# Kernel tuning notes

Hardware: AMD Instinct MI355X
Metric: run time of the kernel (lower is better)

The kernel has to match this reference:

```python
import jax, jax.numpy as jnp
import numpy as np

N = 50000      # num nodes
IN = 256       # in_channels
H = 4          # heads
C = 64         # out_channels per head (concat=False -> out_dim = C)
HOPS = 3       # max_hops == num hops provided
E = 400000     # edges per hop
NEG_SLOPE = 0.2


def setup_inputs() -> dict:
    key = jax.random.key(0)
    ks = jax.random.split(key, 10)
    s_in = 1.0 / np.sqrt(IN)
    s_c = 1.0 / np.sqrt(C)
    return {
        "x": jax.random.normal(ks[0], (N, IN), jnp.float32),
        "ei0": jax.random.randint(ks[1], (2, E), 0, N, dtype=jnp.int32),
        "ei1": jax.random.randint(ks[2], (2, E), 0, N, dtype=jnp.int32),
        "ei2": jax.random.randint(ks[3], (2, E), 0, N, dtype=jnp.int32),
        # shared left/right projections (lin_l / lin_r, shared across hops)
        "W_l": jax.random.normal(ks[4], (IN, H * C), jnp.float32) * s_in,
        "b_l": jnp.zeros((H * C,), jnp.float32),
        "W_r": jax.random.normal(ks[5], (IN, H * C), jnp.float32) * s_in,
        "b_r": jnp.zeros((H * C,), jnp.float32),
        # hop-specific attention vectors and output biases
        "att": jax.random.normal(ks[6], (HOPS, H, C), jnp.float32) * s_c,
        "bias": jnp.zeros((HOPS, C), jnp.float32),
        # hop gate (single Linear since gate_hidden=None)
        "W_gate": jax.random.normal(ks[7], (IN, HOPS), jnp.float32) * s_in,
        "b_gate": jnp.zeros((HOPS,), jnp.float32),
    }


def _segment_softmax(logits, seg, n):
    # logits: [E, H], seg: [E] destination node ids
    m = jax.ops.segment_max(logits, seg, num_segments=n)          # [N, H]
    m = jnp.where(jnp.isfinite(m), m, 0.0)                        # empty segments -> 0
    ex = jnp.exp(logits - m[seg])
    s = jax.ops.segment_sum(ex, seg, num_segments=n)              # [N, H]
    return ex / (s[seg] + 1e-16)


def _gatv2_hop(x_l, x_r, edge_index, att_k, bias_k):
    # x_l, x_r: [N, H, C] shared projections; edge_index: [2, Ek]
    src, dst = edge_index[0], edge_index[1]
    s = jax.nn.leaky_relu(x_l[src] + x_r[dst], NEG_SLOPE)         # [Ek, H, C]
    alpha = jnp.einsum("ehc,hc->eh", s, att_k)                    # [Ek, H]
    alpha = _segment_softmax(alpha, dst, N)
    msg = jax.ops.segment_sum(x_l[src] * alpha[..., None], dst, num_segments=N)  # [N, H, C]
    return msg.mean(axis=1) + bias_k                              # concat=False -> head mean, [N, C]


def reference(x, ei0, ei1, ei2, W_l, b_l, W_r, b_r, att, bias, W_gate, b_gate):
    # shared projections computed once
    x_l = (x @ W_l + b_l).reshape(N, H, C)
    x_r = (x @ W_r + b_r).reshape(N, H, C)

    # hop 0 gets self-loops (add_self_loops=True); higher hops do not
    ar = jnp.arange(N, dtype=ei0.dtype)
    ei0_sl = jnp.concatenate([ei0, jnp.stack([ar, ar])], axis=1)
    edges = [ei0_sl, ei1, ei2]

    messages = jnp.stack(
        [_gatv2_hop(x_l, x_r, edges[k], att[k], bias[k]) for k in range(HOPS)],
        axis=1,
    )  # [N, HOPS, C]

    logits = x @ W_gate + b_gate                                  # [N, HOPS]
    weights = jax.nn.softmax(logits, axis=-1)
    out = jnp.einsum("nkc,nk->nc", messages, weights)             # [N, C]
    return out
```

## Files before the change

kernel.cpp:

```cpp
#include <hip/hip_runtime.h>
#include <math.h>

#define N_NODES 50000
#define IN_DIM 256
#define HEADS 4
#define CDIM 64
#define HC 256
#define HOPS 3
#define EDGES 400000
#define NEG_SLOPE 0.2f
#define SEG (EDGES + N_NODES)
#define TOT_E (3 * EDGES + N_NODES)
#define CAP 40

#define NB_GATE  ((N_NODES + 3) / 4)
#define NB_PACKW ((IN_DIM * 2 * HC) / 256)
#define NB_SCAT  ((TOT_E + 255) / 256)
#define GEMM_BX  ((N_NODES + 127) / 128)

typedef unsigned short ushort;
using short8  = __attribute__((ext_vector_type(8))) short;
using floatx4 = __attribute__((ext_vector_type(4))) float;
using f32x2   = __attribute__((ext_vector_type(2))) float;

__device__ __forceinline__ void decode_flat(int f, int& k, int& e)
{
    if (f < SEG)              { k = 0; e = f; }
    else if (f < SEG + EDGES) { k = 1; e = f - SEG; }
    else                      { k = 2; e = f - SEG - EDGES; }
}

__device__ __forceinline__ ushort f2bf(float f)
{
    unsigned u = __float_as_uint(f);
    unsigned r = u + 0x7fffu + ((u >> 16) & 1u);
    return (ushort)(r >> 16);
}

__device__ __forceinline__ f32x2 bf2x(unsigned u)
{
    f32x2 r;
    r.x = __uint_as_float(u << 16);
    r.y = __uint_as_float(u & 0xffff0000u);
    return r;
}

__device__ __forceinline__ f32x2 lrelu2(f32x2 v)
{
    return __builtin_elementwise_max(v, 0.2f * v);
}

__global__ __launch_bounds__(256) void prep(
    const float* __restrict__ X, const float* __restrict__ Wg,
    const float* __restrict__ bg, float* __restrict__ gw,
    ushort* __restrict__ Xb,
    const float* __restrict__ Wl, const float* __restrict__ Wr,
    ushort* __restrict__ WT,
    const int* __restrict__ ei0, const int* __restrict__ ei1,
    const int* __restrict__ ei2, int* __restrict__ cnt,
    int* __restrict__ bucket)
{
    const int blk = blockIdx.x;
    const int tid = threadIdx.x;

    if (blk < NB_GATE) {
        const int node = (blk * 256 + tid) >> 6;
        const int lane = tid & 63;
        if (node >= N_NODES) return;

        float4 xv = ((const float4*)(X + (size_t)node * IN_DIM))[lane];

        union { ushort s[4]; uint2 u; } o;
        o.s[0] = f2bf(xv.x); o.s[1] = f2bf(xv.y);
        o.s[2] = f2bf(xv.z); o.s[3] = f2bf(xv.w);
        ((uint2*)(Xb + (size_t)node * IN_DIM))[lane] = o.u;

        float a0 = 0.f, a1 = 0.f, a2 = 0.f;
        const int i0 = lane * 4;
        a0 += xv.x * Wg[(i0 + 0) * HOPS + 0]; a1 += xv.x * Wg[(i0 + 0) * HOPS + 1]; a2 += xv.x * Wg[(i0 + 0) * HOPS + 2];
        a0 += xv.y * Wg[(i0 + 1) * HOPS + 0]; a1 += xv.y * Wg[(i0 + 1) * HOPS + 1]; a2 += xv.y * Wg[(i0 + 1) * HOPS + 2];
        a0 += xv.z * Wg[(i0 + 2) * HOPS + 0]; a1 += xv.z * Wg[(i0 + 2) * HOPS + 1]; a2 += xv.z * Wg[(i0 + 2) * HOPS + 2];
        a0 += xv.w * Wg[(i0 + 3) * HOPS + 0]; a1 += xv.w * Wg[(i0 + 3) * HOPS + 1]; a2 += xv.w * Wg[(i0 + 3) * HOPS + 2];

        #pragma unroll
        for (int off = 32; off >= 1; off >>= 1) {
            a0 += __shfl_xor(a0, off);
            a1 += __shfl_xor(a1, off);
            a2 += __shfl_xor(a2, off);
        }
        if (lane == 0) {
            float l0 = a0 + bg[0], l1 = a1 + bg[1], l2 = a2 + bg[2];
            float m = fmaxf(l0, fmaxf(l1, l2));
            float e0 = expf(l0 - m), e1 = expf(l1 - m), e2 = expf(l2 - m);
            float inv = 1.f / (e0 + e1 + e2);
            gw[node * HOPS + 0] = e0 * inv;
            gw[node * HOPS + 1] = e1 * inv;
            gw[node * HOPS + 2] = e2 * inv;
        }
    } else if (blk < NB_GATE + NB_PACKW) {
        int id = (blk - NB_GATE) * 256 + tid;
        int n = id >> 8;
        int k = id & 255;
        float v = (n < HC) ? Wl[k * HC + n] : Wr[k * HC + (n - HC)];
        WT[(size_t)n * IN_DIM + k] = f2bf(v);
    } else {
        int f = (blk - NB_GATE - NB_PACKW) * 256 + tid;
        if (f >= TOT_E) return;
        int k, e; decode_flat(f, k, e);
        int s, d;
        if (k == 0 && e >= EDGES) { s = d = e - EDGES; }
        else {
            const int* ei = (k == 0) ? ei0 : (k == 1) ? ei1 : ei2;
            s = ei[e]; d = ei[EDGES + e];
        }
        int pos = atomicAdd(&cnt[k * N_NODES + d], 1);
        if (pos < CAP)
            bucket[((size_t)k * N_NODES + d) * CAP + pos] = s;
    }
}

#define TM 128
#define TN 128
#define TK 32
#define LDP 40

__global__ __launch_bounds__(256) void gemm_mfma(
    const ushort* __restrict__ Xb, const ushort* __restrict__ WT,
    const float* __restrict__ b_l, const float* __restrict__ b_r,
    ushort* __restrict__ xlb, ushort* __restrict__ xrb, int M)
{
    __shared__ ushort As[TM][LDP];
    __shared__ ushort Bs[TN][LDP];
    const int tid  = threadIdx.x;
    const int wave = tid >> 6, lane = tid & 63;
    const int row0 = blockIdx.x * TM;
    const int col0 = blockIdx.y * TN;
    const int wy = (wave >> 1) * 64, wx = (wave & 1) * 64;
    const int lrow = lane & 15, lk = (lane >> 4) * 8;

    floatx4 acc[4][4];
    #pragma unroll
    for (int i = 0; i < 4; i++)
        #pragma unroll
        for (int j = 0; j < 4; j++)
            acc[i][j] = (floatx4){0.f, 0.f, 0.f, 0.f};

    for (int k0 = 0; k0 < IN_DIM; k0 += TK) {
        #pragma unroll
        for (int j = 0; j < 2; j++) {
            int id = tid + 256 * j;
            int r  = id >> 2;
            int c  = (id & 3) * 8;
            int gr = row0 + r;
            uint4 v = make_uint4(0u, 0u, 0u, 0u);
            if (gr < M)
                v = *(const uint4*)(Xb + (size_t)gr * IN_DIM + k0 + c);
            *(uint4*)&As[r][c] = v;
        }
        #pragma unroll
        for (int j = 0; j < 2; j++) {
            int id = tid + 256 * j;
            int r  = id >> 2;
            int c  = (id & 3) * 8;
            *(uint4*)&Bs[r][c] =
                *(const uint4*)(WT + (size_t)(col0 + r) * IN_DIM + k0 + c);
        }
        __syncthreads();

        short8 af[4], bf[4];
        #pragma unroll
        for (int mi = 0; mi < 4; mi++)
            af[mi] = *(const short8*)&As[wy + mi * 16 + lrow][lk];
        #pragma unroll
        for (int ni = 0; ni < 4; ni++)
            bf[ni] = *(const short8*)&Bs[wx + ni * 16 + lrow][lk];

        #pragma unroll
        for (int mi = 0; mi < 4; mi++)
            #pragma unroll
            for (int ni = 0; ni < 4; ni++)
                acc[mi][ni] = __builtin_amdgcn_mfma_f32_16x16x32_bf16(
                    bf[ni], af[mi], acc[mi][ni], 0, 0, 0);
        __syncthreads();
    }

    const int csub = (lane >> 4) * 4;
    #pragma unroll
    for (int mi = 0; mi < 4; mi++) {
        int grow = row0 + wy + mi * 16 + lrow;
        if (grow < M) {
            #pragma unroll
            for (int ni = 0; ni < 4; ni++) {
                int gcol = col0 + wx + ni * 16 + csub;
                floatx4 v = acc[mi][ni];
                const bool left = (gcol < HC);
                const float4 b = left ? *(const float4*)(b_l + gcol)
                                      : *(const float4*)(b_r + gcol - HC);
                union { ushort s[4]; uint2 u; } o;
                o.s[0] = f2bf(v[0] + b.x);
                o.s[1] = f2bf(v[1] + b.y);
                o.s[2] = f2bf(v[2] + b.z);
                o.s[3] = f2bf(v[3] + b.w);
                ushort* dst = left ? (xlb + (size_t)grow * HC + gcol)
                                   : (xrb + (size_t)grow * HC + gcol - HC);
                *(uint2*)dst = o.u;
            }
        }
    }
}

__global__ __launch_bounds__(256) void node_all(
    const ushort* __restrict__ xlb, const ushort* __restrict__ xrb,
    const int* __restrict__ cnt, const int* __restrict__ bucket,
    const float* __restrict__ att, const float* __restrict__ gw,
    const float* __restrict__ bias, float* __restrict__ out)
{
    const int n    = blockIdx.x * 4 + (threadIdx.x >> 6);
    const int lane = threadIdx.x & 63;
    if (n >= N_NODES) return;
    const int half = lane >> 5;
    const int sub  = lane & 31;
    const unsigned laneoff = (unsigned)sub * 8;

    uint4 rq = *(const uint4*)(xrb + (size_t)n * HC + laneoff);
    f32x2 rr[4] = { bf2x(rq.x), bf2x(rq.y), bf2x(rq.z), bf2x(rq.w) };

    f32x2 outacc[4] = { {0.f,0.f}, {0.f,0.f}, {0.f,0.f}, {0.f,0.f} };

    #pragma unroll
    for (int k = 0; k < HOPS; ++k) {
        const int deg = min(cnt[k * N_NODES + n], CAP);
        const int* bk = bucket + ((size_t)k * N_NODES + n) * CAP;

        const float4 a0 = ((const float4*)(att + (size_t)k * HC))[sub * 2 + 0];
        const float4 a1 = ((const float4*)(att + (size_t)k * HC))[sub * 2 + 1];
        f32x2 w2[4] = { {a0.x, a0.y}, {a0.z, a0.w}, {a1.x, a1.y}, {a1.z, a1.w} };

        float denom = 0.f;
        f32x2 acc2[4] = { {0.f,0.f}, {0.f,0.f}, {0.f,0.f}, {0.f,0.f} };

        if (deg > 0) {
            const int degm1 = deg - 1;
            int myS = (lane < deg) ? bk[lane] : 0;
            const int npair = (deg + 1) >> 1;

            int s0 = __shfl(myS, min(half, degm1));
            uint4 q = *(const uint4*)(xlb + (unsigned)s0 * HC + laneoff);

            for (int j = 0; j < npair; j++) {
                int sn = __shfl(myS, min(2 * (j + 1) + half, degm1));
                uint4 qn = *(const uint4*)(xlb + (unsigned)sn * HC + laneoff);

                f32x2 f0 = bf2x(q.x), f1 = bf2x(q.y);
                f32x2 f2 = bf2x(q.z), f3 = bf2x(q.w);

                f32x2 pp = w2[0] * lrelu2(f0 + rr[0]);
                pp = __builtin_elementwise_fma(w2[1], lrelu2(f1 + rr[1]), pp);
                pp = __builtin_elementwise_fma(w2[2], lrelu2(f2 + rr[2]), pp);
                pp = __builtin_elementwise_fma(w2[3], lrelu2(f3 + rr[3]), pp);
                float p = pp.x + pp.y;

                p += __shfl_xor(p, 1);
                p += __shfl_xor(p, 2);
                p += __shfl_xor(p, 4);

                bool valid = (2 * j + half) < deg;
                float ex = valid ? __expf(p) : 0.f;
                denom += ex;
                f32x2 ex2 = { ex, ex };
                acc2[0] = __builtin_elementwise_fma(ex2, f0, acc2[0]);
                acc2[1] = __builtin_elementwise_fma(ex2, f1, acc2[1]);
                acc2[2] = __builtin_elementwise_fma(ex2, f2, acc2[2]);
                acc2[3] = __builtin_elementwise_fma(ex2, f3, acc2[3]);
                q = qn;
            }
        }

        denom += __shfl_xor(denom, 32);
        const float inv = (denom > 0.f) ? 1.f / denom : 0.f;
        #pragma unroll
        for (int i = 0; i < 4; i++) {
            acc2[i].x += __shfl_xor(acc2[i].x, 32);
            acc2[i].y += __shfl_xor(acc2[i].y, 32);
            acc2[i].x *= inv;
            acc2[i].y *= inv;
            acc2[i].x += __shfl_xor(acc2[i].x, 8);
            acc2[i].y += __shfl_xor(acc2[i].y, 8);
            acc2[i].x += __shfl_xor(acc2[i].x, 16);
            acc2[i].y += __shfl_xor(acc2[i].y, 16);
        }

        const float g   = gw[n * HOPS + k];
        const float s   = g * 0.25f;
        const f32x2 s2  = { s, s };
        const f32x2 g2  = { g, g };
        const f32x2* bb2 =
            (const f32x2*)(bias + (size_t)k * CDIM + (size_t)(sub & 7) * 8);
        #pragma unroll
        for (int i = 0; i < 4; i++) {
            outacc[i] = __builtin_elementwise_fma(s2, acc2[i], outacc[i]);
            outacc[i] = __builtin_elementwise_fma(g2, bb2[i], outacc[i]);
        }
    }

    if (lane < 8) {
        float4 o0 = { outacc[0].x, outacc[0].y, outacc[1].x, outacc[1].y };
        float4 o1 = { outacc[2].x, outacc[2].y, outacc[3].x, outacc[3].y };
        float4* dst = (float4*)(out + (size_t)n * CDIM + (size_t)lane * 8);
        dst[0] = o0;
        dst[1] = o1;
    }
}

extern "C" void kernel_launch(void* const* d_in, const int* in_sizes, int n_in,
                              void* d_out, int out_size, void* d_ws, size_t ws_size,
                              hipStream_t stream)
{
    const float* x      = (const float*)d_in[0];
    const int*   ei0    = (const int*)d_in[1];
    const int*   ei1    = (const int*)d_in[2];
    const int*   ei2    = (const int*)d_in[3];
    const float* W_l    = (const float*)d_in[4];
    const float* b_l    = (const float*)d_in[5];
    const float* W_r    = (const float*)d_in[6];
    const float* b_r    = (const float*)d_in[7];
    const float* att    = (const float*)d_in[8];
    const float* bias   = (const float*)d_in[9];
    const float* W_gate = (const float*)d_in[10];
    const float* b_gate = (const float*)d_in[11];

    const size_t NHC = (size_t)N_NODES * HC;
    float* ws      = (float*)d_ws;
    float* gwbuf   = ws;
    int*   cnt     = (int*)(gwbuf + HOPS * N_NODES);
    int*   bucket  = cnt + HOPS * N_NODES;
    ushort* xlb    = (ushort*)(bucket + (size_t)HOPS * N_NODES * CAP);
    ushort* xrb    = xlb + NHC;
    ushort* Xb     = xrb + NHC;
    ushort* WT     = Xb + NHC;

    hipMemsetAsync(cnt, 0, (size_t)HOPS * N_NODES * sizeof(int), stream);

    prep<<<NB_GATE + NB_PACKW + NB_SCAT, 256, 0, stream>>>(
        x, W_gate, b_gate, gwbuf, Xb, W_l, W_r, WT,
        ei0, ei1, ei2, cnt, bucket);

    dim3 ggrid(GEMM_BX, 4);
    gemm_mfma<<<ggrid, 256, 0, stream>>>(Xb, WT, b_l, b_r, xlb, xrb, N_NODES);

    node_all<<<(N_NODES + 3) / 4, 256, 0, stream>>>(
        xlb, xrb, cnt, bucket, att, gwbuf, bias, (float*)d_out);
}
```

Baseline: 406.4 us.

## Split node aggregation across hops: one wave per hop, combine via LDS

The per-node kernel now launches one 192-thread block per node, with each of the three waves handling one hop's attention and aggregation in parallel instead of looping over hops serially within one wave. Per-hop gated results are written to shared memory and summed after a block barrier, then stored with one coalesced write per node. This shortens each wave's dependent gather chain and exposes more memory-level parallelism. The cost is a block barrier, more blocks, a redundant load of the right-projection row in every wave, and uneven work when hop degrees differ.

```diff
diff --git a/kernel.cpp b/kernel.cpp
--- a/kernel.cpp
+++ b/kernel.cpp
@@ -209,107 +209,95 @@
     }
 }
 
-__global__ __launch_bounds__(256) void node_all(
+__global__ __launch_bounds__(192) void node_all(
     const ushort* __restrict__ xlb, const ushort* __restrict__ xrb,
     const int* __restrict__ cnt, const int* __restrict__ bucket,
     const float* __restrict__ att, const float* __restrict__ gw,
     const float* __restrict__ bias, float* __restrict__ out)
 {
-    const int n    = blockIdx.x * 4 + (threadIdx.x >> 6);
+    __shared__ float lds[HOPS][CDIM];
+    const int n    = blockIdx.x;
+    const int k    = threadIdx.x >> 6;
     const int lane = threadIdx.x & 63;
-    if (n >= N_NODES) return;
     const int half = lane >> 5;
     const int sub  = lane & 31;
     const unsigned laneoff = (unsigned)sub * 8;
 
+    const int deg = min(cnt[k * N_NODES + n], CAP);
+    const int* bk = bucket + ((size_t)k * N_NODES + n) * CAP;
+
     uint4 rq = *(const uint4*)(xrb + (size_t)n * HC + laneoff);
     f32x2 rr[4] = { bf2x(rq.x), bf2x(rq.y), bf2x(rq.z), bf2x(rq.w) };
 
-    f32x2 outacc[4] = { {0.f,0.f}, {0.f,0.f}, {0.f,0.f}, {0.f,0.f} };
+    const float4 a0 = ((const float4*)(att + (size_t)k * HC))[sub * 2 + 0];
+    const float4 a1 = ((const float4*)(att + (size_t)k * HC))[sub * 2 + 1];
+    f32x2 w2[4] = { {a0.x, a0.y}, {a0.z, a0.w}, {a1.x, a1.y}, {a1.z, a1.w} };
+
+    float denom = 0.f;
+    f32x2 acc2[4] = { {0.f,0.f}, {0.f,0.f}, {0.f,0.f}, {0.f,0.f} };
+
+    if (deg > 0) {
+        const int degm1 = deg - 1;
+        int myS = (lane < deg) ? bk[lane] : 0;
+        const int npair = (deg + 1) >> 1;
+
+        int s0 = __shfl(myS, min(half, degm1));
+        uint4 q = *(const uint4*)(xlb + (unsigned)s0 * HC + laneoff);
+
+        for (int j = 0; j < npair; j++) {
+            int sn = __shfl(myS, min(2 * (j + 1) + half, degm1));
+            uint4 qn = *(const uint4*)(xlb + (unsigned)sn * HC + laneoff);
+
+            f32x2 f0 = bf2x(q.x), f1 = bf2x(q.y);
+            f32x2 f2 = bf2x(q.z), f3 = bf2x(q.w);
+
+            f32x2 pp = w2[0] * lrelu2(f0 + rr[0]);
+            pp = __builtin_elementwise_fma(w2[1], lrelu2(f1 + rr[1]), pp);
+            pp = __builtin_elementwise_fma(w2[2], lrelu2(f2 + rr[2]), pp);
+            pp = __builtin_elementwise_fma(w2[3], lrelu2(f3 + rr[3]), pp);
+            float p = pp.x + pp.y;
+
+            p += __shfl_xor(p, 1);
+            p += __shfl_xor(p, 2);
+            p += __shfl_xor(p, 4);
+
+            bool valid = (2 * j + half) < deg;
+            float ex = valid ? __expf(p) : 0.f;
+            denom += ex;
+            f32x2 ex2 = { ex, ex };
+            acc2[0] = __builtin_elementwise_fma(ex2, f0, acc2[0]);
+            acc2[1] = __builtin_elementwise_fma(ex2, f1, acc2[1]);
+            acc2[2] = __builtin_elementwise_fma(ex2, f2, acc2[2]);
+            acc2[3] = __builtin_elementwise_fma(ex2, f3, acc2[3]);
+            q = qn;
+        }
+    }
+
+    denom += __shfl_xor(denom, 32);
+    const float inv = (denom > 0.f) ? 1.f / denom : 0.f;
+    const float g   = gw[n * HOPS + k];
+    const float* bb = bias + (size_t)k * CDIM + (size_t)(sub & 7) * 8;
 
     #pragma unroll
-    for (int k = 0; k < HOPS; ++k) {
-        const int deg = min(cnt[k * N_NODES + n], CAP);
-        const int* bk = bucket + ((size_t)k * N_NODES + n) * CAP;
-
-        const float4 a0 = ((const float4*)(att + (size_t)k * HC))[sub * 2 + 0];
-        const float4 a1 = ((const float4*)(att + (size_t)k * HC))[sub * 2 + 1];
-        f32x2 w2[4] = { {a0.x, a0.y}, {a0.z, a0.w}, {a1.x, a1.y}, {a1.z, a1.w} };
-
-        float denom = 0.f;
-        f32x2 acc2[4] = { {0.f,0.f}, {0.f,0.f}, {0.f,0.f}, {0.f,0.f} };
-
-        if (deg > 0) {
-            const int degm1 = deg - 1;
-            int myS = (lane < deg) ? bk[lane] : 0;
-            const int npair = (deg + 1) >> 1;
-
-            int s0 = __shfl(myS, min(half, degm1));
-            uint4 q = *(const uint4*)(xlb + (unsigned)s0 * HC + laneoff);
-
-            for (int j = 0; j < npair; j++) {
-                int sn = __shfl(myS, min(2 * (j + 1) + half, degm1));
-                uint4 qn = *(const uint4*)(xlb + (unsigned)sn * HC + laneoff);
-
-                f32x2 f0 = bf2x(q.x), f1 = bf2x(q.y);
-                f32x2 f2 = bf2x(q.z), f3 = bf2x(q.w);
-
-                f32x2 pp = w2[0] * lrelu2(f0 + rr[0]);
-                pp = __builtin_elementwise_fma(w2[1], lrelu2(f1 + rr[1]), pp);
-                pp = __builtin_elementwise_fma(w2[2], lrelu2(f2 + rr[2]), pp);
-                pp = __builtin_elementwise_fma(w2[3], lrelu2(f3 + rr[3]), pp);
-                float p = pp.x + pp.y;
-
-                p += __shfl_xor(p, 1);
-                p += __shfl_xor(p, 2);
-                p += __shfl_xor(p, 4);
-
-                bool valid = (2 * j + half) < deg;
-                float ex = valid ? __expf(p) : 0.f;
-                denom += ex;
-                f32x2 ex2 = { ex, ex };
-                acc2[0] = __builtin_elementwise_fma(ex2, f0, acc2[0]);
-                acc2[1] = __builtin_elementwise_fma(ex2, f1, acc2[1]);
-                acc2[2] = __builtin_elementwise_fma(ex2, f2, acc2[2]);
-                acc2[3] = __builtin_elementwise_fma(ex2, f3, acc2[3]);
-                q = qn;
-            }
-        }
-
-        denom += __shfl_xor(denom, 32);
-        const float inv = (denom > 0.f) ? 1.f / denom : 0.f;
-        #pragma unroll
-        for (int i = 0; i < 4; i++) {
-            acc2[i].x += __shfl_xor(acc2[i].x, 32);
-            acc2[i].y += __shfl_xor(acc2[i].y, 32);
-            acc2[i].x *= inv;
-            acc2[i].y *= inv;
-            acc2[i].x += __shfl_xor(acc2[i].x, 8);
-            acc2[i].y += __shfl_xor(acc2[i].y, 8);
-            acc2[i].x += __shfl_xor(acc2[i].x, 16);
-            acc2[i].y += __shfl_xor(acc2[i].y, 16);
-        }
-
-        const float g   = gw[n * HOPS + k];
-        const float s   = g * 0.25f;
-        const f32x2 s2  = { s, s };
-        const f32x2 g2  = { g, g };
-        const f32x2* bb2 =
-            (const f32x2*)(bias + (size_t)k * CDIM + (size_t)(sub & 7) * 8);
-        #pragma unroll
-        for (int i = 0; i < 4; i++) {
-            outacc[i] = __builtin_elementwise_fma(s2, acc2[i], outacc[i]);
-            outacc[i] = __builtin_elementwise_fma(g2, bb2[i], outacc[i]);
-        }
-    }
-
-    if (lane < 8) {
-        float4 o0 = { outacc[0].x, outacc[0].y, outacc[1].x, outacc[1].y };
-        float4 o1 = { outacc[2].x, outacc[2].y, outacc[3].x, outacc[3].y };
-        float4* dst = (float4*)(out + (size_t)n * CDIM + (size_t)lane * 8);
-        dst[0] = o0;
-        dst[1] = o1;
-    }
+    for (int i = 0; i < 4; i++) {
+        acc2[i].x += __shfl_xor(acc2[i].x, 32);
+        acc2[i].y += __shfl_xor(acc2[i].y, 32);
+        acc2[i].x *= inv;
+        acc2[i].y *= inv;
+        acc2[i].x += __shfl_xor(acc2[i].x, 8);
+        acc2[i].y += __shfl_xor(acc2[i].y, 8);
+        acc2[i].x += __shfl_xor(acc2[i].x, 16);
+        acc2[i].y += __shfl_xor(acc2[i].y, 16);
+        if (lane < 8) {
+            lds[k][lane * 8 + 2 * i]     = g * (acc2[i].x * 0.25f + bb[2 * i]);
+            lds[k][lane * 8 + 2 * i + 1] = g * (acc2[i].y * 0.25f + bb[2 * i + 1]);
+        }
+    }
+    __syncthreads();
+
+    if (threadIdx.x < CDIM)
+        out[(size_t)n * CDIM + threadIdx.x] =
+            lds[0][threadIdx.x] + lds[1][threadIdx.x] + lds[2][threadIdx.x];
 }
 
 extern "C" void kernel_launch(void* const* d_in, const int* in_sizes, int n_in,
@@ -348,6 +336,6 @@
     dim3 ggrid(GEMM_BX, 4);
     gemm_mfma<<<ggrid, 256, 0, stream>>>(Xb, WT, b_l, b_r, xlb, xrb, N_NODES);
 
-    node_all<<<(N_NODES + 3) / 4, 256, 0, stream>>>(
+    node_all<<<N_NODES, 192, 0, stream>>>(
         xlb, xrb, cnt, bucket, att, gwbuf, bias, (float*)d_out);
 }
```

Result: faster. 377.6 us (-7.1%).
